# Optimization experiments

Measured on AMD Instinct MI355X. Metric: run time of the kernel, lower is better.

## Reference

```python
import jax, jax.numpy as jnp
import numpy as np
from jax.scipy.special import gammaln, logsumexp

N = 524288      # batch of points on the sphere
D = 512         # x_dim
REG = 1e-6      # kappa regularizer (vMF.__init__ default-style reg)
K_TERMS = 512   # series terms for log I_s(kappa); plenty for kappa ~ O(1..10)


def log_bessel_i(s, kappa, n_terms=K_TERMS):
    """log I_s(kappa) via the ascending series, stably in log-space.
    I_s(x) = sum_k (x/2)^{2k+s} / (k! * Gamma(k+s+1)).
    Replaces the original's CPU mpmath.besseli round-trip."""
    k = jnp.arange(n_terms, dtype=kappa.dtype)
    log_terms = (2.0 * k + s) * jnp.log(kappa / 2.0) - gammaln(k + 1.0) - gammaln(k + s + 1.0)
    return logsumexp(log_terms)


def setup_inputs() -> dict:
    key = jax.random.key(0)
    k1, k2, k3 = jax.random.split(key, 3)
    x = jax.random.normal(k1, (N, D), dtype=jnp.float32)
    x = x / jnp.linalg.norm(x, axis=1, keepdims=True)  # unit-norm rows (vMF support)
    mu_unnorm = jax.random.normal(k2, (D,), dtype=jnp.float32)
    logkappa = jax.random.uniform(k3, (1,), dtype=jnp.float32)
    return {"x": x, "mu_unnorm": mu_unnorm, "logkappa": logkappa}


def reference(x, mu_unnorm, logkappa):
    d = x.shape[1]
    # mu property: mu_unnorm / ||mu_unnorm||
    mu = mu_unnorm / jnp.linalg.norm(mu_unnorm)
    # kappa property: exp(logkappa) + reg
    kappa = jnp.exp(logkappa[0]) + REG
    s = 0.5 * d - 1.0
    # dotp = (mu.unsqueeze(0) * x).sum(1)  -> [N]
    dotp = x @ mu
    # logC = d * (-0.5*log(2*pi)) + s*log(kappa) - log I_s(kappa)
    nhlog2pi = -0.5 * jnp.log(2.0 * jnp.pi)
    logI = log_bessel_i(jnp.asarray(s, x.dtype), kappa)
    logC = d * nhlog2pi + s * jnp.log(kappa) - logI
    # logliks = kappa * dotp + logC
    return kappa * dotp + logC
```

## Files before the change

kernel.cpp:

```cpp
#include <hip/hip_runtime.h>

#define VMF_D 512

__global__ void vmf_prep(const float* __restrict__ mu_unnorm,
                         const float* __restrict__ logkappa,
                         float* __restrict__ ws) {
    __shared__ double dred[8];
    __shared__ float  fred[8];
    const int tid  = threadIdx.x;
    const int lane = tid & 63;
    const int wid  = tid >> 6;

    float v  = mu_unnorm[tid];
    float sq = v * v;
    #pragma unroll
    for (int off = 32; off; off >>= 1) sq += __shfl_xor(sq, off);
    if (lane == 0) fred[wid] = sq;
    __syncthreads();
    float norm2 = 0.f;
    #pragma unroll
    for (int i = 0; i < 8; ++i) norm2 += fred[i];
    ws[tid] = v / sqrtf(norm2);

    const double kappa = exp((double)logkappa[0]) + 1e-6;
    const double s     = 0.5 * VMF_D - 1.0;
    const double lh    = log(kappa * 0.5);
    double lt = (2.0 * tid + s) * lh
              - lgamma((double)tid + 1.0)
              - lgamma((double)tid + s + 1.0);

    double m = lt;
    #pragma unroll
    for (int off = 32; off; off >>= 1) m = fmax(m, __shfl_xor(m, off));
    if (lane == 0) dred[wid] = m;
    __syncthreads();
    double mall = dred[0];
    #pragma unroll
    for (int i = 1; i < 8; ++i) mall = fmax(mall, dred[i]);

    double e = exp(lt - mall);
    #pragma unroll
    for (int off = 32; off; off >>= 1) e += __shfl_xor(e, off);
    __syncthreads();
    if (lane == 0) dred[wid] = e;
    __syncthreads();

    if (tid == 0) {
        double ssum = 0.0;
        for (int i = 0; i < 8; ++i) ssum += dred[i];
        double logI = mall + log(ssum);
        double logC = (double)VMF_D * -0.91893853320467274178
                    + s * log(kappa) - logI;
        ws[VMF_D]     = (float)kappa;
        ws[VMF_D + 1] = (float)logC;
    }
}

__global__ void __launch_bounds__(256)
vmf_main(const float* __restrict__ x,
         const float* __restrict__ ws,
         float* __restrict__ out,
         int n) {
    const int lane   = threadIdx.x & 63;
    const int wave   = (blockIdx.x * blockDim.x + threadIdx.x) >> 6;
    const int nwaves = (gridDim.x * blockDim.x) >> 6;

    const float4 m0 = *reinterpret_cast<const float4*>(ws + lane * 4);
    const float4 m1 = *reinterpret_cast<const float4*>(ws + 256 + lane * 4);
    const float kappa = ws[VMF_D];
    const float logC  = ws[VMF_D + 1];

    for (int row = wave; row < n; row += nwaves) {
        const float* xr = x + (size_t)row * VMF_D;
        const float4 a0 = *reinterpret_cast<const float4*>(xr + lane * 4);
        const float4 a1 = *reinterpret_cast<const float4*>(xr + 256 + lane * 4);
        float p = a0.x * m0.x + a0.y * m0.y + a0.z * m0.z + a0.w * m0.w
                + a1.x * m1.x + a1.y * m1.y + a1.z * m1.z + a1.w * m1.w;
        #pragma unroll
        for (int off = 32; off; off >>= 1) p += __shfl_xor(p, off);
        if (lane == 0) out[row] = fmaf(kappa, p, logC);
    }
}

extern "C" void kernel_launch(void* const* d_in, const int* in_sizes, int n_in,
                              void* d_out, int out_size, void* d_ws, size_t ws_size,
                              hipStream_t stream) {
    const float* x         = (const float*)d_in[0];
    const float* mu_unnorm = (const float*)d_in[1];
    const float* logkappa  = (const float*)d_in[2];
    float* out = (float*)d_out;
    float* ws  = (float*)d_ws;
    const int n = in_sizes[0] / VMF_D;

    vmf_prep<<<1, VMF_D, 0, stream>>>(mu_unnorm, logkappa, ws);
    vmf_main<<<2048, 256, 0, stream>>>(x, ws, out, n);
}
```

Baseline: 210.7 us.

## Process four rows per wave with nontemporal loads and vectorized output stores

The main kernel now has each wave handle a group of four consecutive rows. It issues eight 16-byte nontemporal loads up front and interleaves the four shuffle reductions, so more memory requests are in flight per wave. Results go out as one nontemporal float4 store, the grid doubles to 4096 blocks, and launch bounds request 8 blocks per SM. A tail loop covers leftover rows, at the cost of more registers per thread.

```diff
diff --git a/kernel.cpp b/kernel.cpp
--- a/kernel.cpp
+++ b/kernel.cpp
@@ -1,6 +1,8 @@
 #include <hip/hip_runtime.h>
 
 #define VMF_D 512
+
+typedef float f32x4 __attribute__((ext_vector_type(4)));
 
 __global__ void vmf_prep(const float* __restrict__ mu_unnorm,
                          const float* __restrict__ logkappa,
@@ -56,7 +58,7 @@
     }
 }
 
-__global__ void __launch_bounds__(256)
+__global__ void __launch_bounds__(256, 8)
 vmf_main(const float* __restrict__ x,
          const float* __restrict__ ws,
          float* __restrict__ out,
@@ -65,20 +67,55 @@
     const int wave   = (blockIdx.x * blockDim.x + threadIdx.x) >> 6;
     const int nwaves = (gridDim.x * blockDim.x) >> 6;
 
-    const float4 m0 = *reinterpret_cast<const float4*>(ws + lane * 4);
-    const float4 m1 = *reinterpret_cast<const float4*>(ws + 256 + lane * 4);
+    const f32x4 m0 = *reinterpret_cast<const f32x4*>(ws + lane * 4);
+    const f32x4 m1 = *reinterpret_cast<const f32x4*>(ws + 256 + lane * 4);
     const float kappa = ws[VMF_D];
     const float logC  = ws[VMF_D + 1];
 
-    for (int row = wave; row < n; row += nwaves) {
-        const float* xr = x + (size_t)row * VMF_D;
-        const float4 a0 = *reinterpret_cast<const float4*>(xr + lane * 4);
-        const float4 a1 = *reinterpret_cast<const float4*>(xr + 256 + lane * 4);
-        float p = a0.x * m0.x + a0.y * m0.y + a0.z * m0.z + a0.w * m0.w
-                + a1.x * m1.x + a1.y * m1.y + a1.z * m1.z + a1.w * m1.w;
+    const int ngroups = n >> 2;
+    for (int g = wave; g < ngroups; g += nwaves) {
+        const float* xr = x + ((size_t)g << 11);
+        f32x4 a0[4], a1[4];
         #pragma unroll
-        for (int off = 32; off; off >>= 1) p += __shfl_xor(p, off);
-        if (lane == 0) out[row] = fmaf(kappa, p, logC);
+        for (int r = 0; r < 4; ++r) {
+            a0[r] = __builtin_nontemporal_load(
+                        reinterpret_cast<const f32x4*>(xr + r * VMF_D + lane * 4));
+            a1[r] = __builtin_nontemporal_load(
+                        reinterpret_cast<const f32x4*>(xr + r * VMF_D + 256 + lane * 4));
+        }
+        float p[4];
+        #pragma unroll
+        for (int r = 0; r < 4; ++r) {
+            p[r] = a0[r].x * m0.x + a0[r].y * m0.y + a0[r].z * m0.z + a0[r].w * m0.w
+                 + a1[r].x * m1.x + a1[r].y * m1.y + a1[r].z * m1.z + a1[r].w * m1.w;
+        }
+        #pragma unroll
+        for (int off = 32; off; off >>= 1) {
+            #pragma unroll
+            for (int r = 0; r < 4; ++r) p[r] += __shfl_xor(p[r], off);
+        }
+        if (lane == 0) {
+            f32x4 o;
+            o.x = fmaf(kappa, p[0], logC);
+            o.y = fmaf(kappa, p[1], logC);
+            o.z = fmaf(kappa, p[2], logC);
+            o.w = fmaf(kappa, p[3], logC);
+            __builtin_nontemporal_store(o, reinterpret_cast<f32x4*>(out + (g << 2)));
+        }
+    }
+
+    const int tail_start = ngroups << 2;
+    if (wave == nwaves - 1) {
+        for (int row = tail_start; row < n; ++row) {
+            const float* xr = x + (size_t)row * VMF_D;
+            const f32x4 a0 = *reinterpret_cast<const f32x4*>(xr + lane * 4);
+            const f32x4 a1 = *reinterpret_cast<const f32x4*>(xr + 256 + lane * 4);
+            float p = a0.x * m0.x + a0.y * m0.y + a0.z * m0.z + a0.w * m0.w
+                    + a1.x * m1.x + a1.y * m1.y + a1.z * m1.z + a1.w * m1.w;
+            #pragma unroll
+            for (int off = 32; off; off >>= 1) p += __shfl_xor(p, off);
+            if (lane == 0) out[row] = fmaf(kappa, p, logC);
+        }
     }
 }
 
@@ -93,5 +130,5 @@
     const int n = in_sizes[0] / VMF_D;
 
     vmf_prep<<<1, VMF_D, 0, stream>>>(mu_unnorm, logkappa, ws);
-    vmf_main<<<2048, 256, 0, stream>>>(x, ws, out, n);
+    vmf_main<<<4096, 256, 0, stream>>>(x, ws, out, n);
 }
```

Result: faster. 186.5 us (-11.5%).

## Process four rows per wave with double-buffered nontemporal loads

Applied to the files above, without the earlier changes.

Each wave now handles groups of four rows and prefetches the next group into a second register buffer while reducing the current one. Loads and stores use nontemporal hints, and the four results are written as one vector store. The grid is doubled and launch bounds set for occupancy. This aims to keep more memory requests in flight on a bandwidth-bound stream, at the cost of more registers per thread.

```diff
diff --git a/kernel.cpp b/kernel.cpp
--- a/kernel.cpp
+++ b/kernel.cpp
@@ -1,6 +1,8 @@
 #include <hip/hip_runtime.h>
 
 #define VMF_D 512
+
+typedef float f32x4 __attribute__((ext_vector_type(4)));
 
 __global__ void vmf_prep(const float* __restrict__ mu_unnorm,
                          const float* __restrict__ logkappa,
@@ -56,7 +58,44 @@
     }
 }
 
-__global__ void __launch_bounds__(256)
+#define LOADG(BUF0, BUF1, gidx)                                                  \
+    {                                                                            \
+        const float* xr_ = x + ((size_t)(gidx) << 11);         \
+        _Pragma("unroll")                                                        \
+        for (int r = 0; r < 4; ++r) {                                            \
+            BUF0[r] = __builtin_nontemporal_load(                                \
+                reinterpret_cast<const f32x4*>(xr_ + r * VMF_D + lane * 4));     \
+            BUF1[r] = __builtin_nontemporal_load(                                \
+                reinterpret_cast<const f32x4*>(xr_ + r * VMF_D + 256 + lane * 4)); \
+        }                                                                        \
+    }
+
+#define COMPUTE(BUF0, BUF1, gidx)                                                \
+    {                                                                            \
+        float p_[4];                                                             \
+        _Pragma("unroll")                                                        \
+        for (int r = 0; r < 4; ++r)                                              \
+            p_[r] = BUF0[r].x * m0.x + BUF0[r].y * m0.y + BUF0[r].z * m0.z       \
+                  + BUF0[r].w * m0.w                                             \
+                  + BUF1[r].x * m1.x + BUF1[r].y * m1.y + BUF1[r].z * m1.z       \
+                  + BUF1[r].w * m1.w;                                            \
+        _Pragma("unroll")                                                        \
+        for (int off_ = 32; off_; off_ >>= 1) {                                  \
+            _Pragma("unroll")                                                    \
+            for (int r = 0; r < 4; ++r) p_[r] += __shfl_xor(p_[r], off_);        \
+        }                                                                        \
+        if (lane == 0) {                                                         \
+            f32x4 o_;                                                            \
+            o_.x = fmaf(kappa, p_[0], logC);                                     \
+            o_.y = fmaf(kappa, p_[1], logC);                                     \
+            o_.z = fmaf(kappa, p_[2], logC);                                     \
+            o_.w = fmaf(kappa, p_[3], logC);                                     \
+            __builtin_nontemporal_store(                                         \
+                o_, reinterpret_cast<f32x4*>(out + ((size_t)(gidx) << 2)));      \
+        }                                                                        \
+    }
+
+__global__ void __launch_bounds__(256, 4)
 vmf_main(const float* __restrict__ x,
          const float* __restrict__ ws,
          float* __restrict__ out,
@@ -65,20 +104,42 @@
     const int wave   = (blockIdx.x * blockDim.x + threadIdx.x) >> 6;
     const int nwaves = (gridDim.x * blockDim.x) >> 6;
 
-    const float4 m0 = *reinterpret_cast<const float4*>(ws + lane * 4);
-    const float4 m1 = *reinterpret_cast<const float4*>(ws + 256 + lane * 4);
+    const f32x4 m0 = *reinterpret_cast<const f32x4*>(ws + lane * 4);
+    const f32x4 m1 = *reinterpret_cast<const f32x4*>(ws + 256 + lane * 4);
     const float kappa = ws[VMF_D];
     const float logC  = ws[VMF_D + 1];
 
-    for (int row = wave; row < n; row += nwaves) {
-        const float* xr = x + (size_t)row * VMF_D;
-        const float4 a0 = *reinterpret_cast<const float4*>(xr + lane * 4);
-        const float4 a1 = *reinterpret_cast<const float4*>(xr + 256 + lane * 4);
-        float p = a0.x * m0.x + a0.y * m0.y + a0.z * m0.z + a0.w * m0.w
-                + a1.x * m1.x + a1.y * m1.y + a1.z * m1.z + a1.w * m1.w;
-        #pragma unroll
-        for (int off = 32; off; off >>= 1) p += __shfl_xor(p, off);
-        if (lane == 0) out[row] = fmaf(kappa, p, logC);
+    const int ngroups = n >> 2;
+    f32x4 A0[4], A1[4], B0[4], B1[4];
+
+    int g = wave;
+    if (g < ngroups) {
+        LOADG(A0, A1, g);
+        while (true) {
+            const int g1 = g + nwaves;
+            if (g1 < ngroups) LOADG(B0, B1, g1);
+            COMPUTE(A0, A1, g);
+            if (g1 >= ngroups) break;
+            const int g2 = g1 + nwaves;
+            if (g2 < ngroups) LOADG(A0, A1, g2);
+            COMPUTE(B0, B1, g1);
+            if (g2 >= ngroups) break;
+            g = g2;
+        }
+    }
+
+    const int tail_start = ngroups << 2;
+    if (wave == nwaves - 1) {
+        for (int row = tail_start; row < n; ++row) {
+            const float* xr = x + (size_t)row * VMF_D;
+            const f32x4 a0 = *reinterpret_cast<const f32x4*>(xr + lane * 4);
+            const f32x4 a1 = *reinterpret_cast<const f32x4*>(xr + 256 + lane * 4);
+            float p = a0.x * m0.x + a0.y * m0.y + a0.z * m0.z + a0.w * m0.w
+                    + a1.x * m1.x + a1.y * m1.y + a1.z * m1.z + a1.w * m1.w;
+            #pragma unroll
+            for (int off = 32; off; off >>= 1) p += __shfl_xor(p, off);
+            if (lane == 0) out[row] = fmaf(kappa, p, logC);
+        }
     }
 }
 
@@ -93,5 +154,5 @@
     const int n = in_sizes[0] / VMF_D;
 
     vmf_prep<<<1, VMF_D, 0, stream>>>(mu_unnorm, logkappa, ws);
-    vmf_main<<<2048, 256, 0, stream>>>(x, ws, out, n);
+    vmf_main<<<4096, 256, 0, stream>>>(x, ws, out, n);
 }
```

Result: faster. 178.5 us (-15.3%).
